# Kernel tuning notes

Hardware: AMD Instinct MI355X
Metric: run time of the kernel (lower is better)

## Reference

```python
import jax, jax.numpy as jnp
import numpy as np

N, E, G, H, L, GD = 100000, 1600000, 64, 128, 3, 32
NEG_SLOPE = 0.2
EPS = 1e-5


def setup_inputs() -> dict:
    key = jax.random.key(0)
    ks = jax.random.split(key, 10)
    s = 1.0 / np.sqrt(H)
    return {
        "x": jax.random.normal(ks[0], (N, H), jnp.float32),
        "global_feat": jax.random.normal(ks[1], (G, GD), jnp.float32),
        "W_src": jax.random.normal(ks[2], (L, H, H), jnp.float32) * s,
        "W_dst": jax.random.normal(ks[3], (L, H, H), jnp.float32) * s,
        "att": jax.random.normal(ks[4], (L, H), jnp.float32) * s,
        "b_conv": jnp.zeros((L, H), jnp.float32),
        "gn_w": jnp.ones((L, H), jnp.float32),
        "gn_b": jnp.zeros((L, H), jnp.float32),
        "gn_ms": jnp.ones((L, H), jnp.float32),
        "W1": jax.random.normal(ks[5], (H * L + GD, H), jnp.float32) * (1.0 / np.sqrt(H * L + GD)),
        "b1": jnp.zeros((H,), jnp.float32),
        "W2": jax.random.normal(ks[6], (H, 1), jnp.float32) * s,
        "b2": jnp.zeros((1,), jnp.float32),
        "edge_index": jax.random.randint(ks[7], (2, E), 0, N, jnp.int64),
        "batch": jnp.sort(jax.random.randint(ks[8], (N,), 0, G, jnp.int64)),
    }


def reference(x, global_feat, W_src, W_dst, att, b_conv, gn_w, gn_b, gn_ms,
              W1, b1, W2, b2, edge_index, batch):
    n = x.shape[0]
    g = global_feat.shape[0]
    layers = W_src.shape[0]
    loops = jnp.arange(n, dtype=edge_index.dtype)
    src = jnp.concatenate([edge_index[0], loops])  # add_self_loops=True
    dst = jnp.concatenate([edge_index[1], loops])
    counts = jnp.maximum(
        jax.ops.segment_sum(jnp.ones((n,), x.dtype), batch, num_segments=g), 1.0)

    outs = []
    for l in range(layers):
        # --- GATv2Conv (heads=1) ---
        xl = x @ W_src[l]          # source transform [N,H]
        xr = x @ W_dst[l]          # target transform [N,H]
        e = jax.nn.leaky_relu(xl[src] + xr[dst], NEG_SLOPE) @ att[l]  # [Etot]
        emax = jax.ops.segment_max(e, dst, num_segments=n)
        ex = jnp.exp(e - emax[dst])
        denom = jax.ops.segment_sum(ex, dst, num_segments=n)
        alpha = ex / denom[dst]
        h = jax.ops.segment_sum(alpha[:, None] * xl[src], dst, num_segments=n) + b_conv[l]
        # --- GraphNorm ---
        mean = jax.ops.segment_sum(h, batch, num_segments=g) / counts[:, None]
        sub = h - gn_ms[l] * mean[batch]
        var = jax.ops.segment_sum(sub * sub, batch, num_segments=g) / counts[:, None]
        h = gn_w[l] * sub * jax.lax.rsqrt(var[batch] + EPS) + gn_b[l]
        x = jax.nn.relu(h)
        # --- global_mean_pool ---
        outs.append(jax.ops.segment_sum(x, batch, num_segments=g) / counts[:, None])

    hcat = jnp.concatenate(outs + [global_feat], axis=1)  # JK cat + global feats
    z = jax.nn.relu(hcat @ W1 + b1)  # dropout = identity (eval)
    return z @ W2 + b2
```

## Files before the change

kernel.cpp:

```cpp
#include <hip/hip_runtime.h>
#include <hip/hip_bf16.h>
#include <math.h>

#define N_    100000
#define E_    1600000
#define ETOT_ 1700000
#define G_    64
#define H_    128
#define GH_   8192
#define L_    3
#define GD_   32
#define NEG_  0.2f
#define EPS_  1e-5f

#define NBUK_ 391
#define CH_   2048
#define MCH_  782

typedef unsigned short ushort_t;
typedef unsigned int uint_t;
typedef __attribute__((ext_vector_type(4))) float f32x4;
typedef __attribute__((ext_vector_type(8))) short bf16x8;
typedef __attribute__((ext_vector_type(8))) unsigned short ushort8;

__device__ __forceinline__ ushort_t bfb(float f) {
    __hip_bfloat16 h = __float2bfloat16(f);
    return *reinterpret_cast<ushort_t*>(&h);
}
__device__ __forceinline__ float uf(ushort_t u) {
    return __uint_as_float(((uint_t)u) << 16);
}


__global__ void k_init(float* pooled, float* gsum, float* gsq, int* gstart,
                       const int* __restrict__ batch) {
    int i = blockIdx.x * 256 + threadIdx.x;
    if (i < L_ * GH_) { pooled[i] = 0.f; gsum[i] = 0.f; gsq[i] = 0.f; }
    if (i <= G_) {
        int lo = 0, hi = N_;
        while (lo < hi) { int mid = (lo + hi) >> 1; if (batch[mid] < i) lo = mid + 1; else hi = mid; }
        gstart[i] = lo;
    }
}


__global__ __launch_bounds__(256) void k_bcount(const int* __restrict__ edst, int* __restrict__ C) {
    __shared__ int hist[NBUK_];
    int t = threadIdx.x, m = blockIdx.x;
    for (int i = t; i < NBUK_; i += 256) hist[i] = 0;
    __syncthreads();
    int base = m * CH_;
#pragma unroll
    for (int j = 0; j < CH_ / 256; j++) {
        int e = base + j * 256 + t;
        if (e < E_) atomicAdd(&hist[edst[e] >> 8], 1);
    }
    __syncthreads();
    for (int i = t; i < NBUK_; i += 256) C[i * MCH_ + m] = hist[i];
}

__global__ __launch_bounds__(1024) void k_bscan(int* __restrict__ C, int* __restrict__ bucketEdges) {
    __shared__ int arr[1024];
    int b = blockIdx.x, t = threadIdx.x;
    int v = (t < MCH_) ? C[b * MCH_ + t] : 0;
    arr[t] = v;
    __syncthreads();
    for (int off = 1; off < 1024; off <<= 1) {
        int x = (t >= off) ? arr[t - off] : 0;
        __syncthreads();
        arr[t] += x;
        __syncthreads();
    }
    if (t < MCH_) C[b * MCH_ + t] = arr[t] - v;
    if (t == 1023) bucketEdges[b] = arr[1023];
}

__global__ __launch_bounds__(512) void k_bscan2(const int* __restrict__ bucketEdges,
                                                int* __restrict__ bstartE, int* __restrict__ bstartT,
                                                int* __restrict__ rowptr) {
    __shared__ int aE[512], aT[512];
    int t = threadIdx.x;
    int e = 0, tot = 0;
    if (t < NBUK_) {
        e = bucketEdges[t];
        int nib = N_ - t * 256; if (nib > 256) nib = 256;
        tot = e + nib;
    }
    aE[t] = e; aT[t] = tot;
    __syncthreads();
    for (int off = 1; off < 512; off <<= 1) {
        int xe = (t >= off) ? aE[t - off] : 0;
        int xt = (t >= off) ? aT[t - off] : 0;
        __syncthreads();
        aE[t] += xe; aT[t] += xt;
        __syncthreads();
    }
    if (t < NBUK_) { bstartE[t] = aE[t] - e; bstartT[t] = aT[t] - tot; }
    if (t == 0) rowptr[N_] = ETOT_;
}

__global__ __launch_bounds__(256) void k_bscatter(const int* __restrict__ esrc, const int* __restrict__ edst,
                                                  const int* __restrict__ C, const int* __restrict__ bstartE,
                                                  int2* __restrict__ stag) {
    __shared__ int cur[NBUK_];
    int t = threadIdx.x, m = blockIdx.x;
    for (int i = t; i < NBUK_; i += 256) cur[i] = C[i * MCH_ + m] + bstartE[i];
    __syncthreads();
    int base = m * CH_;
#pragma unroll
    for (int j = 0; j < CH_ / 256; j++) {
        int e = base + j * 256 + t;
        if (e < E_) {
            int s = esrc[e], d = edst[e];
            int pos = atomicAdd(&cur[d >> 8], 1);
            int2 p; p.x = s; p.y = d;
            stag[pos] = p;
        }
    }
}

__global__ __launch_bounds__(256) void k_bfinal(const int2* __restrict__ stag,
                                                const int* __restrict__ bucketEdges,
                                                const int* __restrict__ bstartE, const int* __restrict__ bstartT,
                                                int* __restrict__ rowptr, int* __restrict__ colarr) {
    __shared__ int deg[256];
    __shared__ int cursor[256];
    int b = blockIdx.x, t = threadIdx.x;
    int nb0 = b * 256;
    int nib = N_ - nb0; if (nib > 256) nib = 256;
    int ebeg = bstartE[b], ecnt = bucketEdges[b];
    deg[t] = (t < nib) ? 1 : 0;
    __syncthreads();
    for (int i = t; i < ecnt; i += 256) {
        int2 p = stag[ebeg + i];
        atomicAdd(&deg[p.y - nb0], 1);
    }
    __syncthreads();
    int v = deg[t];
    cursor[t] = v;
    __syncthreads();
    for (int off = 1; off < 256; off <<= 1) {
        int x = (t >= off) ? cursor[t - off] : 0;
        __syncthreads();
        cursor[t] += x;
        __syncthreads();
    }
    int excl = cursor[t] - v;
    int rowbase = bstartT[b];
    if (t < nib) {
        rowptr[nb0 + t] = rowbase + excl;
        colarr[rowbase + excl] = nb0 + t;
    }
    __syncthreads();
    cursor[t] = excl + 1;
    __syncthreads();
    for (int i = t; i < ecnt; i += 256) {
        int2 p = stag[ebeg + i];
        int pos = atomicAdd(&cursor[p.y - nb0], 1);
        colarr[rowbase + pos] = p.x;
    }
}


__global__ void k_prep_w(const float* __restrict__ Ws, const float* __restrict__ Wd,
                         ushort_t* __restrict__ Wt) {
    int i = blockIdx.x * 256 + threadIdx.x;
    if (i >= L_ * 256 * H_) return;
    int l = i >> 15;
    int r = i & 32767;
    int c = r >> 7, k = r & 127;
    float v = (c < H_) ? Ws[(size_t)l * H_ * H_ + k * H_ + c]
                       : Wd[(size_t)l * H_ * H_ + k * H_ + (c - H_)];
    Wt[i] = bfb(v);
}


template<int FIRST>
__global__ __launch_bounds__(256) void k_mfma_t(const float* __restrict__ x0,
                                                const ushort_t* __restrict__ hin,
                                                const int* __restrict__ batch,
                                                const float* __restrict__ mv,
                                                const float* __restrict__ iv,
                                                const float* __restrict__ bb,
                                                const ushort_t* __restrict__ Wt,
                                                ushort_t* __restrict__ xlb,
                                                ushort_t* __restrict__ xrb) {
    int wv = threadIdx.x >> 6, lane = threadIdx.x & 63;
    int row0 = (blockIdx.x * 4 + wv) * 16;
    if (row0 >= N_) return;
    int sl = lane & 15, q = lane >> 4;
    int row = row0 + sl;

    bf16x8 a[4];
    if (FIRST) {
        const float* ap = x0 + (size_t)row * H_ + q * 8;
#pragma unroll
        for (int kk = 0; kk < 4; kk++) {
            float4 v0 = *(const float4*)(ap + kk * 32);
            float4 v1 = *(const float4*)(ap + kk * 32 + 4);
            bf16x8 t;
            t[0] = (short)bfb(v0.x); t[1] = (short)bfb(v0.y);
            t[2] = (short)bfb(v0.z); t[3] = (short)bfb(v0.w);
            t[4] = (short)bfb(v1.x); t[5] = (short)bfb(v1.y);
            t[6] = (short)bfb(v1.z); t[7] = (short)bfb(v1.w);
            a[kk] = t;
        }
    } else {
        int g = batch[row];
        const ushort_t* hp = hin + (size_t)row * H_ + q * 8;
        const float* mvp = mv + g * H_ + q * 8;
        const float* ivp = iv + g * H_ + q * 8;
        const float* bbp = bb + q * 8;
#pragma unroll
        for (int kk = 0; kk < 4; kk++) {
            ushort8 u = *(const ushort8*)(hp + kk * 32);
            float4 m0 = *(const float4*)(mvp + kk * 32);
            float4 m1 = *(const float4*)(mvp + kk * 32 + 4);
            float4 i0 = *(const float4*)(ivp + kk * 32);
            float4 i1 = *(const float4*)(ivp + kk * 32 + 4);
            float4 c0 = *(const float4*)(bbp + kk * 32);
            float4 c1 = *(const float4*)(bbp + kk * 32 + 4);
            bf16x8 t;
            t[0] = (short)bfb(fmaxf((uf(u[0]) - m0.x) * i0.x + c0.x, 0.f));
            t[1] = (short)bfb(fmaxf((uf(u[1]) - m0.y) * i0.y + c0.y, 0.f));
            t[2] = (short)bfb(fmaxf((uf(u[2]) - m0.z) * i0.z + c0.z, 0.f));
            t[3] = (short)bfb(fmaxf((uf(u[3]) - m0.w) * i0.w + c0.w, 0.f));
            t[4] = (short)bfb(fmaxf((uf(u[4]) - m1.x) * i1.x + c1.x, 0.f));
            t[5] = (short)bfb(fmaxf((uf(u[5]) - m1.y) * i1.y + c1.y, 0.f));
            t[6] = (short)bfb(fmaxf((uf(u[6]) - m1.z) * i1.z + c1.z, 0.f));
            t[7] = (short)bfb(fmaxf((uf(u[7]) - m1.w) * i1.w + c1.w, 0.f));
            a[kk] = t;
        }
    }

    f32x4 acc[16];
#pragma unroll
    for (int c = 0; c < 16; c++) acc[c] = (f32x4){0.f, 0.f, 0.f, 0.f};

#pragma unroll
    for (int c = 0; c < 16; c++) {
        const ushort_t* bp = Wt + (size_t)(c * 16 + sl) * H_ + q * 8;
#pragma unroll
        for (int kk = 0; kk < 4; kk++) {
            bf16x8 b = *(const bf16x8*)(bp + kk * 32);
            acc[c] = __builtin_amdgcn_mfma_f32_16x16x32_bf16(a[kk], b, acc[c], 0, 0, 0);
        }
    }

    int orow = row0 + q * 4;
#pragma unroll
    for (int c = 0; c < 8; c++)
#pragma unroll
        for (int j = 0; j < 4; j++)
            xlb[(size_t)(orow + j) * H_ + c * 16 + sl] = bfb(acc[c][j]);
#pragma unroll
    for (int c = 8; c < 16; c++)
#pragma unroll
        for (int j = 0; j < 4; j++)
            xrb[(size_t)(orow + j) * H_ + (c - 8) * 16 + sl] = bfb(acc[c][j]);
}


__global__ __launch_bounds__(256) void k_conv(const ushort_t* __restrict__ xlb,
                                              const ushort_t* __restrict__ xrb,
                                              const int* __restrict__ rowptr, const int* __restrict__ colarr,
                                              const float* __restrict__ attl, const float* __restrict__ bcl,
                                              ushort_t* __restrict__ h) {
    int tid = threadIdx.x;
    int lane = tid & 63, wv = tid >> 6;
    int sl = lane & 15, q = lane >> 4;
    int row = blockIdx.x * 16 + wv * 4 + q;
    int d0 = sl * 8;

    float xrv[8], av[8], av5[8];
    {
        ushort8 ux = *(const ushort8*)(xrb + (size_t)row * H_ + d0);
        float4 a0 = *(const float4*)(attl + d0);
        float4 a1 = *(const float4*)(attl + d0 + 4);
        av[0] = a0.x; av[1] = a0.y; av[2] = a0.z; av[3] = a0.w;
        av[4] = a1.x; av[5] = a1.y; av[6] = a1.z; av[7] = a1.w;
#pragma unroll
        for (int e = 0; e < 8; e++) { xrv[e] = uf(ux[e]); av5[e] = NEG_ * av[e]; }
    }

    int jb = rowptr[row];
    int n = rowptr[row + 1] - jb;
    int last = n - 1;

    float ssum = 0.f;
    float ac[8] = {0.f, 0.f, 0.f, 0.f, 0.f, 0.f, 0.f, 0.f};

    int c0 = colarr[jb];
    int c1 = colarr[jb + (1 < last ? 1 : last)];
    int sc = colarr[jb + (2 < last ? 2 : last)];
    ushort8 u0 = *(const ushort8*)(xlb + (size_t)c0 * H_ + d0);
    ushort8 u1 = *(const ushort8*)(xlb + (size_t)c1 * H_ + d0);

    for (int i = 0; i < n; i++) {
        int i3 = i + 3; if (i3 > last) i3 = last;
        int cn = colarr[jb + i3];
        ushort8 u2 = *(const ushort8*)(xlb + (size_t)sc * H_ + d0);

        float v[8];
        float p = 0.f;
#pragma unroll
        for (int e = 0; e < 8; e++) {
            v[e] = uf(u0[e]);
            float t = v[e] + xrv[e];
            p = fmaf(t, (t > 0.f ? av[e] : av5[e]), p);
        }
        p += __shfl_xor(p, 8);
        p += __shfl_xor(p, 4);
        p += __shfl_xor(p, 2);
        p += __shfl_xor(p, 1);
        float wgt = __expf(p);
        ssum += wgt;
#pragma unroll
        for (int e = 0; e < 8; e++) ac[e] = fmaf(wgt, v[e], ac[e]);

        u0 = u1; u1 = u2; sc = cn;
    }

    float inv = 1.f / ssum;
    float4 b0 = *(const float4*)(bcl + d0);
    float4 b1 = *(const float4*)(bcl + d0 + 4);
    ushort8 ho;
    ho[0] = bfb(ac[0] * inv + b0.x); ho[1] = bfb(ac[1] * inv + b0.y);
    ho[2] = bfb(ac[2] * inv + b0.z); ho[3] = bfb(ac[3] * inv + b0.w);
    ho[4] = bfb(ac[4] * inv + b1.x); ho[5] = bfb(ac[5] * inv + b1.y);
    ho[6] = bfb(ac[6] * inv + b1.z); ho[7] = bfb(ac[7] * inv + b1.w);
    *(ushort8*)(h + (size_t)row * H_ + d0) = ho;
}


__global__ void k_gn_stat(const ushort_t* __restrict__ h, const int* __restrict__ batch,
                          float* gsum, float* gsq) {
    int tid = threadIdx.x;
    int nb = blockIdx.x * 64;
    int d2 = (tid & 63) * 2, hh = tid >> 6;
    int nend = nb + 64; if (nend > N_) nend = N_;
    float s10 = 0.f, s11 = 0.f, s20 = 0.f, s21 = 0.f; int curg = -1;
    for (int n = nb + hh; n < nend; n += 4) {
        int g = batch[n];
        if (g != curg) {
            if (curg >= 0) {
                atomicAdd(&gsum[curg * H_ + d2], s10);
                atomicAdd(&gsum[curg * H_ + d2 + 1], s11);
                atomicAdd(&gsq[curg * H_ + d2], s20);
                atomicAdd(&gsq[curg * H_ + d2 + 1], s21);
            }
            s10 = s11 = s20 = s21 = 0.f; curg = g;
        }
        uint_t u = *(const uint_t*)(h + (size_t)n * H_ + d2);
        float v0 = __uint_as_float(u << 16);
        float v1 = __uint_as_float(u & 0xffff0000u);
        s10 += v0; s11 += v1; s20 += v0 * v0; s21 += v1 * v1;
    }
    if (curg >= 0) {
        atomicAdd(&gsum[curg * H_ + d2], s10);
        atomicAdd(&gsum[curg * H_ + d2 + 1], s11);
        atomicAdd(&gsq[curg * H_ + d2], s20);
        atomicAdd(&gsq[curg * H_ + d2 + 1], s21);
    }
}


__global__ void k_gn_fin(float* gsum, float* gsq, const int* __restrict__ gstart,
                         const float* __restrict__ gnwl, const float* __restrict__ gnmsl) {
    int i = blockIdx.x * 256 + threadIdx.x;
    if (i < GH_) {
        int g = i >> 7, d = i & 127;
        int c = gstart[g + 1] - gstart[g]; if (c < 1) c = 1;
        float ic = 1.f / (float)c;
        float mean = gsum[i] * ic;
        float e2   = gsq[i] * ic;
        float ms = gnmsl[d];
        float var = e2 - ms * (2.f - ms) * mean * mean;
        gsum[i] = ms * mean;
        gsq[i]  = gnwl[d] * rsqrtf(var + EPS_);
    }
}


__global__ void k_pool(const ushort_t* __restrict__ h, const int* __restrict__ batch,
                       const float* __restrict__ mv, const float* __restrict__ iv,
                       const float* __restrict__ bb, float* __restrict__ pooled_l) {
    int tid = threadIdx.x;
    int nb = blockIdx.x * 64;
    int d2 = (tid & 63) * 2, hh = tid >> 6;
    int nend = nb + 64; if (nend > N_) nend = N_;
    float b0 = bb[d2], b1 = bb[d2 + 1];
    float p0 = 0.f, p1 = 0.f; int curg = -1;
    float m0 = 0.f, m1 = 0.f, i0 = 0.f, i1 = 0.f;
    for (int n = nb + hh; n < nend; n += 4) {
        int g = batch[n];
        if (g != curg) {
            if (curg >= 0) {
                atomicAdd(&pooled_l[curg * H_ + d2], p0);
                atomicAdd(&pooled_l[curg * H_ + d2 + 1], p1);
            }
            p0 = 0.f; p1 = 0.f; curg = g;
            m0 = mv[g * H_ + d2]; m1 = mv[g * H_ + d2 + 1];
            i0 = iv[g * H_ + d2]; i1 = iv[g * H_ + d2 + 1];
        }
        uint_t u = *(const uint_t*)(h + (size_t)n * H_ + d2);
        float v0 = __uint_as_float(u << 16);
        float v1 = __uint_as_float(u & 0xffff0000u);
        v0 = fmaxf((v0 - m0) * i0 + b0, 0.f);
        v1 = fmaxf((v1 - m1) * i1 + b1, 0.f);
        p0 += v0; p1 += v1;
    }
    if (curg >= 0) {
        atomicAdd(&pooled_l[curg * H_ + d2], p0);
        atomicAdd(&pooled_l[curg * H_ + d2 + 1], p1);
    }
}


__global__ __launch_bounds__(128) void k_mlp(const float* __restrict__ pooled, const float* __restrict__ gfeat,
                                             const int* __restrict__ gstart,
                                             const float* __restrict__ W1, const float* __restrict__ b1,
                                             const float* __restrict__ W2, const float* __restrict__ b2,
                                             float* __restrict__ out) {
    int g = blockIdx.x;
    int c = threadIdx.x;
    __shared__ float hc[H_ * L_ + GD_];
    __shared__ float zz[H_];
    int cn = gstart[g + 1] - gstart[g]; if (cn < 1) cn = 1;
    float ic = 1.f / (float)cn;
    for (int k = c; k < H_ * L_; k += 128)
        hc[k] = pooled[(k >> 7) * GH_ + g * H_ + (k & 127)] * ic;
    if (c < GD_) hc[H_ * L_ + c] = gfeat[g * GD_ + c];
    __syncthreads();
    float z = b1[c];
#pragma unroll 4
    for (int k = 0; k < H_ * L_ + GD_; k++)
        z += hc[k] * W1[k * H_ + c];
    z = fmaxf(z, 0.f);
    zz[c] = z * W2[c];
    __syncthreads();
    for (int off = 64; off > 0; off >>= 1) {
        if (c < off) zz[c] += zz[c + off];
        __syncthreads();
    }
    if (c == 0) out[g] = zz[0] + b2[0];
}


extern "C" void kernel_launch(void* const* d_in, const int* in_sizes, int n_in,
                              void* d_out, int out_size, void* d_ws, size_t ws_size,
                              hipStream_t stream) {
    const float* x0    = (const float*)d_in[0];
    const float* gfeat = (const float*)d_in[1];
    const float* Wsrc  = (const float*)d_in[2];
    const float* Wdst  = (const float*)d_in[3];
    const float* att   = (const float*)d_in[4];
    const float* bconv = (const float*)d_in[5];
    const float* gnw   = (const float*)d_in[6];
    const float* gnb   = (const float*)d_in[7];
    const float* gnms  = (const float*)d_in[8];
    const float* W1    = (const float*)d_in[9];
    const float* b1    = (const float*)d_in[10];
    const float* W2    = (const float*)d_in[11];
    const float* b2    = (const float*)d_in[12];
    const int*   eidx  = (const int*)d_in[13];
    const int*   batch = (const int*)d_in[14];
    const int* esrc = eidx;
    const int* edst = eidx + E_;
    float* out = (float*)d_out;

    char* w = (char*)d_ws;
    size_t off = 0;
    auto alloc = [&](size_t bytes) { char* p = w + off; off += (bytes + 255) & ~(size_t)255; return p; };
    ushort_t* xlb  = (ushort_t*)alloc((size_t)N_ * H_ * 2);
    ushort_t* xrb  = (ushort_t*)alloc((size_t)N_ * H_ * 2);
    ushort_t* h    = (ushort_t*)alloc((size_t)N_ * H_ * 2);
    ushort_t* Wt   = (ushort_t*)alloc((size_t)L_ * 256 * H_ * 2);
    int*   rowptr  = (int*)alloc((size_t)(N_ + 1) * 4);
    int*   colarr  = (int*)alloc((size_t)ETOT_ * 4);
    int*   bktE    = (int*)alloc(NBUK_ * 4);
    int*   bstartE = (int*)alloc(NBUK_ * 4);
    int*   bstartT = (int*)alloc(NBUK_ * 4);
    int*   gstart  = (int*)alloc((G_ + 1) * 4);
    float* gsum    = (float*)alloc((size_t)L_ * GH_ * 4);
    float* gsq     = (float*)alloc((size_t)L_ * GH_ * 4);
    float* pooled  = (float*)alloc((size_t)L_ * GH_ * 4);
    int2* stag = (int2*)xlb;
    int*  C    = (int*)xrb;
    (void)ws_size; (void)in_sizes; (void)n_in; (void)out_size;

    k_init<<<(N_ + 255) / 256, 256, 0, stream>>>(pooled, gsum, gsq, gstart, batch);
    k_bcount<<<MCH_, 256, 0, stream>>>(edst, C);
    k_bscan<<<NBUK_, 1024, 0, stream>>>(C, bktE);
    k_bscan2<<<1, 512, 0, stream>>>(bktE, bstartE, bstartT, rowptr);
    k_bscatter<<<MCH_, 256, 0, stream>>>(esrc, edst, C, bstartE, stag);
    k_bfinal<<<NBUK_, 256, 0, stream>>>(stag, bktE, bstartE, bstartT, rowptr, colarr);
    k_prep_w<<<(L_ * 256 * H_ + 255) / 256, 256, 0, stream>>>(Wsrc, Wdst, Wt);

    int mfma_grid = (N_ / 16 + 3) / 4;
    for (int l = 0; l < L_; l++) {
        if (l == 0)
            k_mfma_t<1><<<mfma_grid, 256, 0, stream>>>(x0, h, batch, gsum, gsq, gnb,
                                                       Wt, xlb, xrb);
        else
            k_mfma_t<0><<<mfma_grid, 256, 0, stream>>>(x0, h, batch,
                                                       gsum + (size_t)(l - 1) * GH_,
                                                       gsq + (size_t)(l - 1) * GH_,
                                                       gnb + (size_t)(l - 1) * H_,
                                                       Wt + (size_t)l * 256 * H_, xlb, xrb);
        k_conv<<<N_ / 16, 256, 0, stream>>>(xlb, xrb, rowptr, colarr,
                                            att + (size_t)l * H_, bconv + (size_t)l * H_, h);
        k_gn_stat<<<(N_ + 63) / 64, 256, 0, stream>>>(h, batch,
                                                      gsum + (size_t)l * GH_, gsq + (size_t)l * GH_);
        k_gn_fin<<<GH_ / 256, 256, 0, stream>>>(gsum + (size_t)l * GH_, gsq + (size_t)l * GH_,
                                                gstart, gnw + (size_t)l * H_, gnms + (size_t)l * H_);
        k_pool<<<(N_ + 63) / 64, 256, 0, stream>>>(h, batch,
                                                   gsum + (size_t)l * GH_, gsq + (size_t)l * GH_,
                                                   gnb + (size_t)l * H_, pooled + (size_t)l * GH_);
    }

    k_mlp<<<G_, 128, 0, stream>>>(pooled, gfeat, gstart, W1, b1, W2, b2, out);
}
```

Measured before the change: 630.6 us.

## Pack staging edges, fuse weight prep, vectorize MFMA stores, dual-accumulate conv

Folds the weight bf16 transpose into the init kernel to drop one launch. Packs each staged edge into a single 32-bit word (source<<8 | low dst byte), halving staging traffic. Swaps the MFMA operand order so each lane holds four consecutive output columns, allowing packed 8-byte stores instead of scattered 2-byte stores. Restructures the GAT aggregation loop into two independent accumulator chains with a shorter prefetch, trading prefetch depth for instruction-level parallelism.

```diff
diff --git a/kernel.cpp b/kernel.cpp
--- a/kernel.cpp
+++ b/kernel.cpp
@@ -27,19 +27,32 @@
     __hip_bfloat16 h = __float2bfloat16(f);
     return *reinterpret_cast<ushort_t*>(&h);
 }
+__device__ __forceinline__ uint_t pack_bf2(float a, float b) {
+    return (uint_t)bfb(a) | ((uint_t)bfb(b) << 16);
+}
 __device__ __forceinline__ float uf(ushort_t u) {
     return __uint_as_float(((uint_t)u) << 16);
 }
 
 
 __global__ void k_init(float* pooled, float* gsum, float* gsq, int* gstart,
-                       const int* __restrict__ batch) {
+                       const int* __restrict__ batch,
+                       const float* __restrict__ Ws, const float* __restrict__ Wd,
+                       ushort_t* __restrict__ Wt) {
     int i = blockIdx.x * 256 + threadIdx.x;
     if (i < L_ * GH_) { pooled[i] = 0.f; gsum[i] = 0.f; gsq[i] = 0.f; }
     if (i <= G_) {
         int lo = 0, hi = N_;
         while (lo < hi) { int mid = (lo + hi) >> 1; if (batch[mid] < i) lo = mid + 1; else hi = mid; }
         gstart[i] = lo;
+    }
+    if (i < L_ * 256 * H_) {
+        int l = i >> 15;
+        int r = i & 32767;
+        int c = r >> 7, k = r & 127;
+        float v = (c < H_) ? Ws[(size_t)l * H_ * H_ + k * H_ + c]
+                           : Wd[(size_t)l * H_ * H_ + k * H_ + (c - H_)];
+        Wt[i] = bfb(v);
     }
 }
 
@@ -101,7 +114,7 @@
 
 __global__ __launch_bounds__(256) void k_bscatter(const int* __restrict__ esrc, const int* __restrict__ edst,
                                                   const int* __restrict__ C, const int* __restrict__ bstartE,
-                                                  int2* __restrict__ stag) {
+                                                  uint_t* __restrict__ stag) {
     __shared__ int cur[NBUK_];
     int t = threadIdx.x, m = blockIdx.x;
     for (int i = t; i < NBUK_; i += 256) cur[i] = C[i * MCH_ + m] + bstartE[i];
@@ -113,13 +126,12 @@
         if (e < E_) {
             int s = esrc[e], d = edst[e];
             int pos = atomicAdd(&cur[d >> 8], 1);
-            int2 p; p.x = s; p.y = d;
-            stag[pos] = p;
-        }
-    }
-}
-
-__global__ __launch_bounds__(256) void k_bfinal(const int2* __restrict__ stag,
+            stag[pos] = ((uint_t)s << 8) | (uint_t)(d & 255);
+        }
+    }
+}
+
+__global__ __launch_bounds__(256) void k_bfinal(const uint_t* __restrict__ stag,
                                                 const int* __restrict__ bucketEdges,
                                                 const int* __restrict__ bstartE, const int* __restrict__ bstartT,
                                                 int* __restrict__ rowptr, int* __restrict__ colarr) {
@@ -132,8 +144,8 @@
     deg[t] = (t < nib) ? 1 : 0;
     __syncthreads();
     for (int i = t; i < ecnt; i += 256) {
-        int2 p = stag[ebeg + i];
-        atomicAdd(&deg[p.y - nb0], 1);
+        uint_t p = stag[ebeg + i];
+        atomicAdd(&deg[p & 255u], 1);
     }
     __syncthreads();
     int v = deg[t];
@@ -155,23 +167,10 @@
     cursor[t] = excl + 1;
     __syncthreads();
     for (int i = t; i < ecnt; i += 256) {
-        int2 p = stag[ebeg + i];
-        int pos = atomicAdd(&cursor[p.y - nb0], 1);
-        colarr[rowbase + pos] = p.x;
-    }
-}
-
-
-__global__ void k_prep_w(const float* __restrict__ Ws, const float* __restrict__ Wd,
-                         ushort_t* __restrict__ Wt) {
-    int i = blockIdx.x * 256 + threadIdx.x;
-    if (i >= L_ * 256 * H_) return;
-    int l = i >> 15;
-    int r = i & 32767;
-    int c = r >> 7, k = r & 127;
-    float v = (c < H_) ? Ws[(size_t)l * H_ * H_ + k * H_ + c]
-                       : Wd[(size_t)l * H_ * H_ + k * H_ + (c - H_)];
-    Wt[i] = bfb(v);
+        uint_t p = stag[ebeg + i];
+        int pos = atomicAdd(&cursor[p & 255u], 1);
+        colarr[rowbase + pos] = (int)(p >> 8);
+    }
 }
 
 
@@ -191,7 +190,7 @@
     int sl = lane & 15, q = lane >> 4;
     int row = row0 + sl;
 
-    bf16x8 a[4];
+    bf16x8 bx[4];
     if (FIRST) {
         const float* ap = x0 + (size_t)row * H_ + q * 8;
 #pragma unroll
@@ -203,7 +202,7 @@
             t[2] = (short)bfb(v0.z); t[3] = (short)bfb(v0.w);
             t[4] = (short)bfb(v1.x); t[5] = (short)bfb(v1.y);
             t[6] = (short)bfb(v1.z); t[7] = (short)bfb(v1.w);
-            a[kk] = t;
+            bx[kk] = t;
         }
     } else {
         int g = batch[row];
@@ -229,7 +228,7 @@
             t[5] = (short)bfb(fmaxf((uf(u[5]) - m1.y) * i1.y + c1.y, 0.f));
             t[6] = (short)bfb(fmaxf((uf(u[6]) - m1.z) * i1.z + c1.z, 0.f));
             t[7] = (short)bfb(fmaxf((uf(u[7]) - m1.w) * i1.w + c1.w, 0.f));
-            a[kk] = t;
+            bx[kk] = t;
         }
     }
 
@@ -239,31 +238,37 @@
 
 #pragma unroll
     for (int c = 0; c < 16; c++) {
-        const ushort_t* bp = Wt + (size_t)(c * 16 + sl) * H_ + q * 8;
+        const ushort_t* wp = Wt + (size_t)(c * 16 + sl) * H_ + q * 8;
 #pragma unroll
         for (int kk = 0; kk < 4; kk++) {
-            bf16x8 b = *(const bf16x8*)(bp + kk * 32);
-            acc[c] = __builtin_amdgcn_mfma_f32_16x16x32_bf16(a[kk], b, acc[c], 0, 0, 0);
-        }
-    }
-
-    int orow = row0 + q * 4;
-#pragma unroll
-    for (int c = 0; c < 8; c++)
-#pragma unroll
-        for (int j = 0; j < 4; j++)
-            xlb[(size_t)(orow + j) * H_ + c * 16 + sl] = bfb(acc[c][j]);
-#pragma unroll
-    for (int c = 8; c < 16; c++)
-#pragma unroll
-        for (int j = 0; j < 4; j++)
-            xrb[(size_t)(orow + j) * H_ + (c - 8) * 16 + sl] = bfb(acc[c][j]);
+            bf16x8 aw = *(const bf16x8*)(wp + kk * 32);
+            acc[c] = __builtin_amdgcn_mfma_f32_16x16x32_bf16(aw, bx[kk], acc[c], 0, 0, 0);
+        }
+    }
+
+    ushort_t* xlp = xlb + (size_t)row * H_ + q * 4;
+    ushort_t* xrp = xrb + (size_t)row * H_ + q * 4;
+#pragma unroll
+    for (int c = 0; c < 8; c++) {
+        uint2 o;
+        o.x = pack_bf2(acc[c][0], acc[c][1]);
+        o.y = pack_bf2(acc[c][2], acc[c][3]);
+        *(uint2*)(xlp + c * 16) = o;
+    }
+#pragma unroll
+    for (int c = 8; c < 16; c++) {
+        uint2 o;
+        o.x = pack_bf2(acc[c][0], acc[c][1]);
+        o.y = pack_bf2(acc[c][2], acc[c][3]);
+        *(uint2*)(xrp + (c - 8) * 16) = o;
+    }
 }
 
 
 __global__ __launch_bounds__(256) void k_conv(const ushort_t* __restrict__ xlb,
                                               const ushort_t* __restrict__ xrb,
-                                              const int* __restrict__ rowptr, const int* __restrict__ colarr,
+                                              const int* __restrict__ rowptr,
+                                              const int* __restrict__ colarr,
                                               const float* __restrict__ attl, const float* __restrict__ bcl,
                                               ushort_t* __restrict__ h) {
     int tid = threadIdx.x;
@@ -285,27 +290,17 @@
 
     int jb = rowptr[row];
     int n = rowptr[row + 1] - jb;
-    int last = n - 1;
-
-    float ssum = 0.f;
-    float ac[8] = {0.f, 0.f, 0.f, 0.f, 0.f, 0.f, 0.f, 0.f};
-
-    int c0 = colarr[jb];
-    int c1 = colarr[jb + (1 < last ? 1 : last)];
-    int sc = colarr[jb + (2 < last ? 2 : last)];
-    ushort8 u0 = *(const ushort8*)(xlb + (size_t)c0 * H_ + d0);
-    ushort8 u1 = *(const ushort8*)(xlb + (size_t)c1 * H_ + d0);
-
-    for (int i = 0; i < n; i++) {
-        int i3 = i + 3; if (i3 > last) i3 = last;
-        int cn = colarr[jb + i3];
-        ushort8 u2 = *(const ushort8*)(xlb + (size_t)sc * H_ + d0);
-
+
+    float ssum0 = 0.f, ssum1 = 0.f;
+    float ac0[8] = {0.f, 0.f, 0.f, 0.f, 0.f, 0.f, 0.f, 0.f};
+    float ac1[8] = {0.f, 0.f, 0.f, 0.f, 0.f, 0.f, 0.f, 0.f};
+
+    auto PROC = [&](const ushort8& u, float& ss, float* acm) {
         float v[8];
         float p = 0.f;
 #pragma unroll
         for (int e = 0; e < 8; e++) {
-            v[e] = uf(u0[e]);
+            v[e] = uf(u[e]);
             float t = v[e] + xrv[e];
             p = fmaf(t, (t > 0.f ? av[e] : av5[e]), p);
         }
@@ -314,21 +309,36 @@
         p += __shfl_xor(p, 2);
         p += __shfl_xor(p, 1);
         float wgt = __expf(p);
-        ssum += wgt;
-#pragma unroll
-        for (int e = 0; e < 8; e++) ac[e] = fmaf(wgt, v[e], ac[e]);
-
-        u0 = u1; u1 = u2; sc = cn;
-    }
-
-    float inv = 1.f / ssum;
+        ss += wgt;
+#pragma unroll
+        for (int e = 0; e < 8; e++) acm[e] = fmaf(wgt, v[e], acm[e]);
+    };
+
+    int cA = colarr[jb];
+    ushort8 uA = *(const ushort8*)(xlb + (size_t)cA * H_ + d0);
+    int cB = colarr[jb + (n > 1 ? 1 : 0)];
+    ushort8 uB = *(const ushort8*)(xlb + (size_t)cB * H_ + d0);
+
+    int i = 0;
+    for (; i + 2 < n; i += 2) {
+        int cC = colarr[jb + i + 2];
+        int cD = colarr[jb + (i + 3 < n ? i + 3 : i + 2)];
+        PROC(uA, ssum0, ac0);
+        uA = *(const ushort8*)(xlb + (size_t)cC * H_ + d0);
+        PROC(uB, ssum1, ac1);
+        uB = *(const ushort8*)(xlb + (size_t)cD * H_ + d0);
+    }
+    PROC(uA, ssum0, ac0);
+    if (i + 1 < n) PROC(uB, ssum1, ac1);
+
+    float inv = 1.f / (ssum0 + ssum1);
     float4 b0 = *(const float4*)(bcl + d0);
     float4 b1 = *(const float4*)(bcl + d0 + 4);
     ushort8 ho;
-    ho[0] = bfb(ac[0] * inv + b0.x); ho[1] = bfb(ac[1] * inv + b0.y);
-    ho[2] = bfb(ac[2] * inv + b0.z); ho[3] = bfb(ac[3] * inv + b0.w);
-    ho[4] = bfb(ac[4] * inv + b1.x); ho[5] = bfb(ac[5] * inv + b1.y);
-    ho[6] = bfb(ac[6] * inv + b1.z); ho[7] = bfb(ac[7] * inv + b1.w);
+    ho[0] = bfb((ac0[0] + ac1[0]) * inv + b0.x); ho[1] = bfb((ac0[1] + ac1[1]) * inv + b0.y);
+    ho[2] = bfb((ac0[2] + ac1[2]) * inv + b0.z); ho[3] = bfb((ac0[3] + ac1[3]) * inv + b0.w);
+    ho[4] = bfb((ac0[4] + ac1[4]) * inv + b1.x); ho[5] = bfb((ac0[5] + ac1[5]) * inv + b1.y);
+    ho[6] = bfb((ac0[6] + ac1[6]) * inv + b1.z); ho[7] = bfb((ac0[7] + ac1[7]) * inv + b1.w);
     *(ushort8*)(h + (size_t)row * H_ + d0) = ho;
 }
 
@@ -485,17 +495,17 @@
     float* gsum    = (float*)alloc((size_t)L_ * GH_ * 4);
     float* gsq     = (float*)alloc((size_t)L_ * GH_ * 4);
     float* pooled  = (float*)alloc((size_t)L_ * GH_ * 4);
-    int2* stag = (int2*)xlb;
-    int*  C    = (int*)xrb;
+    uint_t* stag = (uint_t*)xlb;
+    int*    C    = (int*)xrb;
     (void)ws_size; (void)in_sizes; (void)n_in; (void)out_size;
 
-    k_init<<<(N_ + 255) / 256, 256, 0, stream>>>(pooled, gsum, gsq, gstart, batch);
+    k_init<<<(N_ + 255) / 256, 256, 0, stream>>>(pooled, gsum, gsq, gstart, batch,
+                                                 Wsrc, Wdst, Wt);
     k_bcount<<<MCH_, 256, 0, stream>>>(edst, C);
     k_bscan<<<NBUK_, 1024, 0, stream>>>(C, bktE);
     k_bscan2<<<1, 512, 0, stream>>>(bktE, bstartE, bstartT, rowptr);
     k_bscatter<<<MCH_, 256, 0, stream>>>(esrc, edst, C, bstartE, stag);
     k_bfinal<<<NBUK_, 256, 0, stream>>>(stag, bktE, bstartE, bstartT, rowptr, colarr);
-    k_prep_w<<<(L_ * 256 * H_ + 255) / 256, 256, 0, stream>>>(Wsrc, Wdst, Wt);
 
     int mfma_grid = (N_ / 16 + 3) / 4;
     for (int l = 0; l < L_; l++) {
```

Result: slower. 684.2 us (+8.5%).
